# Optimization experiments

Hardware: AMD Instinct MI355X
Metric: run time of the kernel (lower is better)

The kernel has to match this reference:

```python
import jax, jax.numpy as jnp
import numpy as np

N, D_IN, FC_DIM, GROUP, NONGT, EMB = 4096, 12544, 1024, 16, 300, 64
DG = FC_DIM // GROUP  # 64 per-head dim


def extract_position_matrix(bbox, nongt_dim):
    xmin, ymin, xmax, ymax = jnp.split(bbox, 4, axis=1)  # each [N,1]
    bw = xmax - xmin + 1.0
    bh = ymax - ymin + 1.0
    cx = 0.5 * (xmin + xmax)
    cy = 0.5 * (ymin + ymax)
    dx = jnp.log(jnp.maximum(jnp.abs((cx - cx.T) / bw), 1e-3))
    dy = jnp.log(jnp.maximum(jnp.abs((cy - cy.T) / bh), 1e-3))
    dw = jnp.log(bw / bw.T)
    dh = jnp.log(bh / bh.T)
    # slice to first nongt_dim columns, stack -> [N, nongt, 4]
    return jnp.stack([dx[:, :nongt_dim], dy[:, :nongt_dim],
                      dw[:, :nongt_dim], dh[:, :nongt_dim]], axis=2)


def extract_position_embedding(pos_mat, feat_dim=64, wave_length=1000.0):
    n8 = feat_dim // 8
    feat_range = jnp.arange(n8, dtype=pos_mat.dtype)
    dim_mat = wave_length ** (8.0 / feat_dim * feat_range)  # [8]
    div = 100.0 * pos_mat[..., None] / dim_mat              # [N,nongt,4,8]
    emb = jnp.concatenate([jnp.sin(div), jnp.cos(div)], axis=3)  # [N,nongt,4,16]
    return emb.reshape(pos_mat.shape[0], pos_mat.shape[1], feat_dim)


def attention_multi_head(feat, pos_emb, Wpos, bpos, Wq, bq, Wk, bk, Wo, bo):
    # feat: [N, 1024], pos_emb: [N, nongt, 64]
    nongt_feat = feat[:NONGT]                                   # [nongt, 1024]
    aff_w = jax.nn.relu(pos_emb @ Wpos + bpos)                  # [N, nongt, G]
    aff_w = jnp.swapaxes(aff_w, 1, 2)                           # [N, G, nongt]
    q = (feat @ Wq + bq).reshape(-1, GROUP, DG)                 # [N, G, dg]
    k = (nongt_feat @ Wk + bk).reshape(NONGT, GROUP, DG)        # [nongt, G, dg]
    aff = jnp.einsum('ngd,mgd->ngm', q, k) * (1.0 / np.sqrt(DG))  # [N, G, nongt]
    logits = jnp.log(jnp.maximum(aff_w, 1e-6)) + aff
    p = jax.nn.softmax(logits, axis=2)                          # [N, G, nongt]
    out = jnp.einsum('ngm,mc->ngc', p, nongt_feat)              # [N, G, 1024]
    # grouped 1x1 conv: group g maps 1024 -> 64 outputs
    lin = jnp.einsum('ngc,goc->ngo', out, Wo) + bo.reshape(GROUP, DG)
    return lin.reshape(feat.shape[0], FC_DIM)


def setup_inputs() -> dict:
    key = jax.random.key(0)
    ks = jax.random.split(key, 20)
    roi_feat = jax.random.normal(ks[0], (N, D_IN), dtype=jnp.float32)
    u = jax.random.uniform(ks[1], (N, 4), dtype=jnp.float32)
    x1 = u[:, 0:1] * 500.0
    y1 = u[:, 1:2] * 500.0
    bbox = jnp.concatenate([x1, y1, x1 + u[:, 2:3] * 200.0 + 1.0,
                            y1 + u[:, 3:4] * 200.0 + 1.0], axis=1)
    def lin(k, fin, fout):
        s = 1.0 / np.sqrt(fin)
        return jax.random.normal(k, (fin, fout), dtype=jnp.float32) * s
    inp = {'roi_feat': roi_feat, 'bbox': bbox,
           'W_fc1': lin(ks[2], D_IN, FC_DIM), 'b_fc1': jnp.zeros((FC_DIM,), jnp.float32),
           'W_fc2': lin(ks[3], FC_DIM, FC_DIM), 'b_fc2': jnp.zeros((FC_DIM,), jnp.float32)}
    for i, base in [(1, 4), (2, 10)]:
        inp[f'Wpos{i}'] = lin(ks[base], EMB, GROUP)
        inp[f'bpos{i}'] = jnp.zeros((GROUP,), jnp.float32)
        inp[f'Wq{i}'] = lin(ks[base + 1], FC_DIM, FC_DIM)
        inp[f'bq{i}'] = jnp.zeros((FC_DIM,), jnp.float32)
        inp[f'Wk{i}'] = lin(ks[base + 2], FC_DIM, FC_DIM)
        inp[f'bk{i}'] = jnp.zeros((FC_DIM,), jnp.float32)
        inp[f'Wo{i}'] = jax.random.normal(ks[base + 3], (GROUP, DG, FC_DIM), dtype=jnp.float32) * (1.0 / np.sqrt(FC_DIM))
        inp[f'bo{i}'] = jnp.zeros((FC_DIM,), jnp.float32)
    return inp


def reference(roi_feat, bbox, W_fc1, b_fc1, W_fc2, b_fc2,
              Wpos1, bpos1, Wq1, bq1, Wk1, bk1, Wo1, bo1,
              Wpos2, bpos2, Wq2, bq2, Wk2, bk2, Wo2, bo2):
    pos_mat = extract_position_matrix(bbox, NONGT)
    pos_emb = extract_position_embedding(pos_mat, EMB)
    x = roi_feat
    for (Wf, bf, Wp, bp, Wq, bq, Wk, bk, Wo, bo) in [
        (W_fc1, b_fc1, Wpos1, bpos1, Wq1, bq1, Wk1, bk1, Wo1, bo1),
        (W_fc2, b_fc2, Wpos2, bpos2, Wq2, bq2, Wk2, bk2, Wo2, bo2)]:
        x = x @ Wf + bf
        attn = attention_multi_head(x, pos_emb, Wp, bp, Wq, bq, Wk, bk, Wo, bo)
        x = jax.nn.relu(x + attn)
    return x
```

## Files before the change

### kernel.cpp

```cpp
#include <hip/hip_runtime.h>


using bf16x8 = __attribute__((ext_vector_type(8))) short;
using u16x4  = __attribute__((ext_vector_type(4))) short;
using f32x4  = __attribute__((ext_vector_type(4))) float;
typedef unsigned short u16;
typedef unsigned int   u32;

#define DEV __device__ __forceinline__

DEV u16 f2bf(float f) {
  u32 u = __float_as_uint(f);
  return (u16)((u + 0x7FFFu + ((u >> 16) & 1u)) >> 16);
}
DEV float bf2f(u16 h) { return __uint_as_float(((u32)h) << 16); }

DEV f32x4 mfma16(bf16x8 a, bf16x8 b, f32x4 c) {
  return __builtin_amdgcn_mfma_f32_16x16x32_bf16(a, b, c, 0, 0, 0);
}
DEV void gload16(const u16* g, u16* l) {
  __builtin_amdgcn_global_load_lds((const __attribute__((address_space(1))) void*)g,
                                   (__attribute__((address_space(3))) void*)l, 16, 0, 0);
}

DEV void fsincos(float x, float* s, float* c) {
  float r = x * 0.15915494309189535f;
  r -= rintf(r);
  float a = r * 6.283185307179586f;
  *s = __sinf(a); *c = __cosf(a);
}

struct PrepArgs {
  const float* Wo1; u16* Wo1_b;
  const float* Wo2; u16* Wo2_b;
  const float* Wfc1; u16* Wfc1_t;
  const float* wsrc[5]; u16* wdst[5];
};

__global__ __launch_bounds__(256) void prep_kernel(PrepArgs p) {
  __shared__ float tp[32][36];
  int b = blockIdx.x, tid = threadIdx.x;
  if (b < 1024) {
    const float* src = (b < 512) ? p.Wo1 : p.Wo2;
    u16* dst = (b < 512) ? p.Wo1_b : p.Wo2_b;
    size_t i = ((size_t)(b & 511) * 256 + tid) * 8;
    float4 a = *(const float4*)(src + i);
    float4 c = *(const float4*)(src + i + 4);
    bf16x8 v;
    v[0]=(short)f2bf(a.x); v[1]=(short)f2bf(a.y); v[2]=(short)f2bf(a.z); v[3]=(short)f2bf(a.w);
    v[4]=(short)f2bf(c.x); v[5]=(short)f2bf(c.y); v[6]=(short)f2bf(c.z); v[7]=(short)f2bf(c.w);
    *(bf16x8*)(dst + i) = v;
    return;
  }
  const float* in; u16* out; int r0, c0, R, C;
  if (b < 13568) {
    int idx = b - 1024;
    in = p.Wfc1; out = p.Wfc1_t; R = 12544; C = 1024;
    r0 = (idx >> 5) * 32; c0 = (idx & 31) * 32;
  } else {
    int idx = b - 13568;
    int z = idx >> 10, rest = idx & 1023;
    in = p.wsrc[z]; out = p.wdst[z]; R = 1024; C = 1024;
    r0 = (rest >> 5) * 32; c0 = (rest & 31) * 32;
  }
  {
    int r = tid >> 3, c4 = (tid & 7) * 4;
    float4 v = *(const float4*)(in + (size_t)(r0 + r) * C + c0 + c4);
    *(float4*)&tp[r][c4] = v;
  }
  __syncthreads();
  {
    int c = tid >> 3, r4 = (tid & 7) * 4;
    u16x4 o;
    o[0] = (short)f2bf(tp[r4 + 0][c]); o[1] = (short)f2bf(tp[r4 + 1][c]);
    o[2] = (short)f2bf(tp[r4 + 2][c]); o[3] = (short)f2bf(tp[r4 + 3][c]);
    *(u16x4*)(out + (size_t)(c0 + c) * R + r0 + r4) = o;
  }
}

__global__ __launch_bounds__(512, 2) void gemm8p(
    const float* __restrict__ A, const u16* __restrict__ Bt,
    float* __restrict__ P) {
  const int K = 12544;
  __shared__ u16 lds[65536];
  int tid = threadIdx.x;
  int w = tid >> 6, l = tid & 63, h = l >> 4, l15 = l & 15;
  int wm = w >> 2, wn = w & 3;

  int b = ((blockIdx.x & 7) << 5) | (blockIdx.x >> 3);
  int bz = b >> 6, rest = b & 63;
  int bm = (rest & 15) * 256;
  int bn = (rest >> 4) * 256;
  size_t k0 = (size_t)bz * 3136;

  int arow = tid >> 3;
  int c0 = (tid & 7) * 8;
  const float* pA0 = A + (size_t)(bm + arow) * K + k0 + c0;
  const size_t aseg = (size_t)64 * K;
  int awe = ((arow * 128 + c0 * 2) ^ ((arow & 7) << 4)) >> 1;

  int X = ((tid >> 3) & 7) << 4;
  int lb2 = (tid * 16) ^ X;
  int lr = lb2 >> 7, lc = (lb2 & 127) >> 1;
  const u16* pB = Bt + (size_t)(bn + lr) * K + k0 + lc;
  const size_t o64 = (size_t)64 * K, o128 = (size_t)128 * K, o192 = (size_t)192 * K;

  int swz = (l15 & 7) << 3;
  int xk0 = (h * 8) ^ swz;
  int xk1 = 32 ^ xk0;
  int rA = (wm * 64 + l15) * 64;
  int rB = (wn * 32 + l15) * 64;

  f32x4 acc[8][4];
#pragma unroll
  for (int i = 0; i < 8; i++)
#pragma unroll
    for (int j = 0; j < 4; j++) acc[i][j] = (f32x4){0.f, 0.f, 0.f, 0.f};

  float4 a0[4], a1[4];
  bf16x8 af[4][2], bl[2][2], bh[2][2];

#define AISSUE(kk) { _Pragma("unroll") for (int s = 0; s < 4; s++) {     \
    a0[s] = *(const float4*)(pA0 + s * aseg + (kk));                     \
    a1[s] = *(const float4*)(pA0 + s * aseg + (kk) + 4); } }
#define BISSUE_LO(WB, kk) {                                              \
    gload16(pB + (kk),        (WB) + tid * 8);                           \
    gload16(pB + o64 + (kk),  (WB) + 4096 + tid * 8); }
#define BISSUE_HI(WB, kk) {                                              \
    gload16(pB + o128 + (kk), (WB) + 8192 + tid * 8);                    \
    gload16(pB + o192 + (kk), (WB) + 12288 + tid * 8); }
#define AWRITE(WA) { _Pragma("unroll") for (int s = 0; s < 4; s++) {     \
    bf16x8 v;                                                            \
    v[0]=(short)f2bf(a0[s].x); v[1]=(short)f2bf(a0[s].y);                \
    v[2]=(short)f2bf(a0[s].z); v[3]=(short)f2bf(a0[s].w);                \
    v[4]=(short)f2bf(a1[s].x); v[5]=(short)f2bf(a1[s].y);                \
    v[6]=(short)f2bf(a1[s].z); v[7]=(short)f2bf(a1[s].w);                \
    *(bf16x8*)&(WA)[awe + s * 4096] = v; } }
#define READ_AF(BASE)                                                    \
  _Pragma("unroll") for (int i = 0; i < 4; i++) {                        \
    af[i][0] = *(const bf16x8*)&LA[(BASE) + rA + i * 1024 + xk0];        \
    af[i][1] = *(const bf16x8*)&LA[(BASE) + rA + i * 1024 + xk1];        \
  }
#define READ_BL {                                                        \
  _Pragma("unroll") for (int j = 0; j < 2; j++) {                        \
    bl[j][0] = *(const bf16x8*)&LB[rB + j * 1024 + xk0];                 \
    bl[j][1] = *(const bf16x8*)&LB[rB + j * 1024 + xk1]; } }
#define READ_BH {                                                        \
  _Pragma("unroll") for (int j = 0; j < 2; j++) {                        \
    bh[j][0] = *(const bf16x8*)&LB[8192 + rB + j * 1024 + xk0];          \
    bh[j][1] = *(const bf16x8*)&LB[8192 + rB + j * 1024 + xk1]; } }
#define Q_MFMA(QR, QC, BF)                                               \
  __builtin_amdgcn_s_setprio(1);                                         \
  _Pragma("unroll") for (int i = 0; i < 4; i++)                          \
    _Pragma("unroll") for (int j = 0; j < 2; j++) {                      \
      acc[(QR)*4+i][(QC)*2+j] = mfma16(af[i][0], BF[j][0], acc[(QR)*4+i][(QC)*2+j]); \
      acc[(QR)*4+i][(QC)*2+j] = mfma16(af[i][1], BF[j][1], acc[(QR)*4+i][(QC)*2+j]); \
    }                                                                    \
  __builtin_amdgcn_s_setprio(0);
#define SBAR __builtin_amdgcn_sched_barrier(0)

  AISSUE(0);
  BISSUE_LO(lds + 16384, 0);
  BISSUE_HI(lds + 16384, 0);
  AWRITE(lds);
  asm volatile("s_waitcnt vmcnt(0) lgkmcnt(0)" ::: "memory");
  __builtin_amdgcn_s_barrier();

  for (int t = 0; t < 48; t++) {
    const u16* LA = lds + (t & 1) * 32768;
    const u16* LB = LA + 16384;
    u16* WA = lds + ((t + 1) & 1) * 32768;
    u16* WB = WA + 16384;
    int ktn = (t + 1) * 64;
    AISSUE(ktn);
    asm volatile("s_waitcnt vmcnt(10) lgkmcnt(0)" ::: "memory");
    __builtin_amdgcn_s_barrier();
    SBAR;
    READ_AF(0);
    READ_BL;
    Q_MFMA(0, 0, bl);
    SBAR;
    BISSUE_LO(WB, ktn);
    asm volatile("s_waitcnt vmcnt(10)" ::: "memory");
    __builtin_amdgcn_s_barrier();
    SBAR;
    READ_BH;
    Q_MFMA(0, 1, bh);
    SBAR;
    BISSUE_HI(WB, ktn);
    READ_AF(8192);
    Q_MFMA(1, 1, bh);
    SBAR;
    Q_MFMA(1, 0, bl);
    SBAR;
    AWRITE(WA);
  }
  {
    const u16* LA = lds;
    const u16* LB = lds + 16384;
    asm volatile("s_waitcnt vmcnt(2) lgkmcnt(0)" ::: "memory");
    __builtin_amdgcn_s_barrier();
    SBAR;
    READ_AF(0);
    READ_BL;
    Q_MFMA(0, 0, bl);
    SBAR;
    asm volatile("s_waitcnt vmcnt(0)" ::: "memory");
    __builtin_amdgcn_s_barrier();
    SBAR;
    READ_BH;
    Q_MFMA(0, 1, bh);
    SBAR;
    READ_AF(8192);
    Q_MFMA(1, 1, bh);
    Q_MFMA(1, 0, bl);
  }
#undef AISSUE
#undef BISSUE_LO
#undef BISSUE_HI
#undef AWRITE
#undef READ_AF
#undef READ_BL
#undef READ_BH
#undef Q_MFMA
#undef SBAR

  float* dst = P + (size_t)bz * 4096 * 1024;
#pragma unroll
  for (int qr = 0; qr < 2; qr++)
#pragma unroll
    for (int i = 0; i < 4; i++)
#pragma unroll
      for (int qc = 0; qc < 2; qc++)
#pragma unroll
        for (int j = 0; j < 2; j++) {
          int row0 = bm + qr * 128 + wm * 64 + i * 16 + h * 4;
          int col  = bn + qc * 128 + wn * 32 + j * 16 + l15;
          f32x4 v = acc[qr * 4 + i][qc * 2 + j];
#pragma unroll
          for (int r = 0; r < 4; r++)
            dst[(size_t)(row0 + r) * 1024 + col] = v[r];
        }
}

__constant__ float C100D[8] = {100.f, 42.16965034285822f, 17.78279410038923f,
                               7.498942093324559f, 3.1622776601683795f,
                               1.333521432163324f, 0.5623413251903491f,
                               0.23713737056616552f};

__global__ __launch_bounds__(256) void reduce_pos_kernel(
    const float* __restrict__ P, const float* __restrict__ bias,
    float* __restrict__ xf, u16* __restrict__ xb,
    const float* __restrict__ bbox,
    const float* __restrict__ Wpos1, const float* __restrict__ Wpos2,
    const float* __restrict__ bpos1, const float* __restrict__ bpos2,
    u16* __restrict__ logw1, u16* __restrict__ logw2) {
  __shared__ u16 pool[18944];
  int tid = threadIdx.x;
  if (blockIdx.x < 2048) {
    const size_t MN = (size_t)4096 * 1024;
    size_t i = ((size_t)blockIdx.x * 256 + tid) * 4;
    size_t stride = (size_t)2048 * 256 * 4;
    for (; i < MN; i += stride) {
      float4 a = *(const float4*)(P + i);
      float4 b = *(const float4*)(P + MN + i);
      float4 c = *(const float4*)(P + 2 * MN + i);
      float4 d = *(const float4*)(P + 3 * MN + i);
      float4 bv = *(const float4*)(bias + (i & 1023));
      float4 r;
      r.x = a.x + b.x + c.x + d.x + bv.x;
      r.y = a.y + b.y + c.y + d.y + bv.y;
      r.z = a.z + b.z + c.z + d.z + bv.z;
      r.w = a.w + b.w + c.w + d.w + bv.w;
      *(float4*)(xf + i) = r;
      u16x4 hv;
      hv[0] = (short)f2bf(r.x); hv[1] = (short)f2bf(r.y);
      hv[2] = (short)f2bf(r.z); hv[3] = (short)f2bf(r.w);
      *(u16x4*)(xb + i) = hv;
    }
    return;
  }
  u16* emb_s = pool;
  u16* wp_s  = pool + 5632;
  u16* lw_s  = pool + 8448;
  int n = blockIdx.x - 2048;
  int w = tid >> 6, l = tid & 63, h = l >> 4, l15 = l & 15;
  for (int idx = tid; idx < 1024; idx += 256) {
    int e = idx >> 4, c = idx & 15;
    wp_s[c * 88 + e]        = f2bf(Wpos1[idx]);
    wp_s[(16 + c) * 88 + e] = f2bf(Wpos2[idx]);
  }
  float4 bn = ((const float4*)bbox)[n];
  float bw_n = bn.z - bn.x + 1.f, bh_n = bn.w - bn.y + 1.f;
  float cx_n = 0.5f * (bn.x + bn.z), cy_n = 0.5f * (bn.y + bn.w);
  float bps0 = bpos1[l15], bps1 = bpos2[l15];
  int p = tid >> 2, k = tid & 3;

  for (int m0 = 0; m0 < 320; m0 += 64) {
    int m = m0 + p;
    float4 bm = ((const float4*)bbox)[m];
    float v;
    if (k == 0)      v = logf(fmaxf(fabsf((cx_n - 0.5f * (bm.x + bm.z)) / bw_n), 1e-3f));
    else if (k == 1) v = logf(fmaxf(fabsf((cy_n - 0.5f * (bm.y + bm.w)) / bh_n), 1e-3f));
    else if (k == 2) v = logf(bw_n / (bm.z - bm.x + 1.f));
    else             v = logf(bh_n / (bm.w - bm.y + 1.f));
    __syncthreads();
#pragma unroll
    for (int tt = 0; tt < 8; tt++) {
      float s, c; fsincos(v * C100D[tt], &s, &c);
      emb_s[p * 88 + k * 16 + tt]     = f2bf(s);
      emb_s[p * 88 + k * 16 + 8 + tt] = f2bf(c);
    }
    __syncthreads();
    f32x4 acc0 = {0.f, 0.f, 0.f, 0.f}, acc1 = {0.f, 0.f, 0.f, 0.f};
    bf16x8 a0 = *(const bf16x8*)&emb_s[(w * 16 + l15) * 88 + h * 8];
    bf16x8 a1 = *(const bf16x8*)&emb_s[(w * 16 + l15) * 88 + 32 + h * 8];
    bf16x8 b00 = *(const bf16x8*)&wp_s[l15 * 88 + h * 8];
    bf16x8 b01 = *(const bf16x8*)&wp_s[l15 * 88 + 32 + h * 8];
    bf16x8 b10 = *(const bf16x8*)&wp_s[(16 + l15) * 88 + h * 8];
    bf16x8 b11 = *(const bf16x8*)&wp_s[(16 + l15) * 88 + 32 + h * 8];
    acc0 = mfma16(a0, b00, acc0); acc0 = mfma16(a1, b01, acc0);
    acc1 = mfma16(a0, b10, acc1); acc1 = mfma16(a1, b11, acc1);
#pragma unroll
    for (int r = 0; r < 4; r++) {
      int mm = m0 + w * 16 + h * 4 + r;
      lw_s[l15 * 328 + mm]        = f2bf(logf(fmaxf(acc0[r] + bps0, 1e-6f)));
      lw_s[(16 + l15) * 328 + mm] = f2bf(logf(fmaxf(acc1[r] + bps1, 1e-6f)));
    }
  }
  __syncthreads();
  for (int i = tid; i < 1280; i += 256) {
    int layer = i / 640, rest = i - layer * 640;
    int gg = rest / 40, seg = rest - gg * 40;
    bf16x8 v = *(const bf16x8*)&lw_s[(layer * 16 + gg) * 328 + seg * 8];
    u16* dst = (layer ? logw2 : logw1) + ((size_t)gg * 4096 + n) * 320 + seg * 8;
    *(bf16x8*)dst = v;
  }
}

struct GDesc {
  const u16* A; const u16* Bt; const float* bias;
  u16* Cb; float* Cf;
  int M, N, K, ldc, nt;
};

__global__ __launch_bounds__(256, 2) void gemmU(GDesc g0, GDesc g1, GDesc g2,
                                                int c0, int c1) {
  __shared__ u16 lds[32768];
  GDesc g; int lb = blockIdx.x;
  if (lb < c0) { g = g0; lb = (lb & 7) * (c0 >> 3) + (lb >> 3); }
  else if (lb < c1) { g = g1; lb -= c0; }
  else { g = g2; lb -= c1; }
  int bm = (lb / g.nt) * 128, bn = (lb % g.nt) * 128;
  int tid = threadIdx.x;
  int w = tid >> 6, l = tid & 63, h = l >> 4, l15 = l & 15;
  int wm = w >> 1, wn = w & 1;
  int K = g.K;

  int X = ((tid >> 3) & 7) << 4;
  int lbyte = (tid * 16) ^ X;
  int lr = lbyte >> 7, lc = (lbyte & 127) >> 1;
  const u16 *pa[4], *pb[4];
#pragma unroll
  for (int c = 0; c < 4; c++) {
    pa[c] = g.A  + (size_t)min(bm + c * 32 + lr, g.M - 1) * K + lc;
    pb[c] = g.Bt + (size_t)min(bn + c * 32 + lr, g.N - 1) * K + lc;
  }

  int swz = (l15 & 7) << 3;
  int xk0 = (h * 8) ^ swz;
  int xk1 = 32 ^ xk0;
  int rA = (wm * 64 + l15) * 64;
  int rB = (wn * 64 + l15) * 64;

  f32x4 acc[4][4];
#pragma unroll
  for (int i = 0; i < 4; i++)
#pragma unroll
    for (int j = 0; j < 4; j++) acc[i][j] = (f32x4){0.f, 0.f, 0.f, 0.f};

#define ISSUEU(W, kk)                                     \
  { gload16(pa[0] + (kk), (W) + tid * 8);                 \
    gload16(pa[1] + (kk), (W) + 2048 + tid * 8);          \
    gload16(pa[2] + (kk), (W) + 4096 + tid * 8);          \
    gload16(pa[3] + (kk), (W) + 6144 + tid * 8);          \
    gload16(pb[0] + (kk), (W) + 8192 + tid * 8);          \
    gload16(pb[1] + (kk), (W) + 10240 + tid * 8);         \
    gload16(pb[2] + (kk), (W) + 12288 + tid * 8);         \
    gload16(pb[3] + (kk), (W) + 14336 + tid * 8); }

  ISSUEU(lds, 0);
  int ktiles = K >> 6;
  for (int t = 0; t < ktiles; t++) {
    const u16* LA = lds + (t & 1) * 16384;
    const u16* LB = LA + 8192;
    u16* W = lds + ((t ^ 1) & 1) * 16384;
    if (t < ktiles - 1) {
      ISSUEU(W, (t + 1) * 64);
      asm volatile("s_waitcnt vmcnt(8)" ::: "memory");
    } else {
      asm volatile("s_waitcnt vmcnt(0)" ::: "memory");
    }
    __builtin_amdgcn_s_barrier();
    asm volatile("" ::: "memory");
    bf16x8 a[4][2], bfr[4][2];
#pragma unroll
    for (int i = 0; i < 4; i++) {
      a[i][0] = *(const bf16x8*)&LA[rA + i * 1024 + xk0];
      a[i][1] = *(const bf16x8*)&LA[rA + i * 1024 + xk1];
    }
#pragma unroll
    for (int j = 0; j < 4; j++) {
      bfr[j][0] = *(const bf16x8*)&LB[rB + j * 1024 + xk0];
      bfr[j][1] = *(const bf16x8*)&LB[rB + j * 1024 + xk1];
    }
    __builtin_amdgcn_s_setprio(1);
#pragma unroll
    for (int i = 0; i < 4; i++)
#pragma unroll
      for (int j = 0; j < 4; j++) {
        acc[i][j] = mfma16(a[i][0], bfr[j][0], acc[i][j]);
        acc[i][j] = mfma16(a[i][1], bfr[j][1], acc[i][j]);
      }
    __builtin_amdgcn_s_setprio(0);
    asm volatile("" ::: "memory");
    __builtin_amdgcn_s_barrier();
  }
#undef ISSUEU

#pragma unroll
  for (int i = 0; i < 4; i++) {
#pragma unroll
    for (int j = 0; j < 4; j++) {
      int col = bn + wn * 64 + j * 16 + l15;
      if (col >= g.ldc) continue;
      float bv = (g.bias != nullptr && col < g.N) ? g.bias[col] : 0.f;
      int row0 = bm + wm * 64 + i * 16 + h * 4;
#pragma unroll
      for (int r = 0; r < 4; r++) {
        int row = row0 + r;
        if (row >= g.M) continue;
        float v = acc[i][j][r] + bv;
        size_t off = (size_t)row * g.ldc + col;
        g.Cb[off] = f2bf(v);
        if (g.Cf != nullptr) g.Cf[off] = v;
      }
    }
  }
}

template <bool LAST>
__global__ __launch_bounds__(256) void attn_kernel(
    const u16* __restrict__ qb, const u16* __restrict__ kb,
    const u16* __restrict__ kvt, const u16* __restrict__ logw,
    const float* __restrict__ xf, const float* __restrict__ bo,
    float* __restrict__ outf, u16* __restrict__ outb) {
  __shared__ u16 ps[64 * 344];
  int tid = threadIdx.x;
  int g = blockIdx.y, n0 = blockIdx.x * 64;
  int w = tid >> 6, l = tid & 63, h = l >> 4, l15 = l & 15;

  {
    const u16* src = logw + ((size_t)g * 4096 + n0) * 320;
    for (int i = tid; i < 64 * 40; i += 256) {
      int row = i / 40, seg = i - row * 40;
      *(bf16x8*)&ps[row * 328 + seg * 8] = *(const bf16x8*)(src + row * 320 + seg * 8);
    }
  }
  int nrow = n0 + w * 16 + l15;
  const u16* qp = qb + (size_t)nrow * 1024 + g * 64;
  bf16x8 aq0 = *(const bf16x8*)(qp + h * 8);
  bf16x8 aq1 = *(const bf16x8*)(qp + 32 + h * 8);

  f32x4 acc[19];
#pragma unroll
  for (int f = 0; f < 19; f++) acc[f] = (f32x4){0.f, 0.f, 0.f, 0.f};
  const u16* kp = kb + g * 64 + h * 8;
#pragma unroll
  for (int f = 0; f < 19; f++) {
    bf16x8 b0 = *(const bf16x8*)(kp + (size_t)(f * 16 + l15) * 1024);
    bf16x8 b1 = *(const bf16x8*)(kp + (size_t)(f * 16 + l15) * 1024 + 32);
    acc[f] = mfma16(aq0, b0, acc[f]);
    acc[f] = mfma16(aq1, b1, acc[f]);
  }
  __syncthreads();

  int nbase = n0 + w * 16 + h * 4;
  int lrow = w * 16 + h * 4;
  float mx[4] = {-INFINITY, -INFINITY, -INFINITY, -INFINITY};
  float sm[4] = {0.f, 0.f, 0.f, 0.f};
#pragma unroll
  for (int f = 0; f < 19; f++) {
    int m = f * 16 + l15;
#pragma unroll
    for (int r = 0; r < 4; r++) {
      float lw = -INFINITY;
      if (m < 300) lw = bf2f(ps[(lrow + r) * 328 + m]);
      float lg = acc[f][r] * 0.125f + lw;
      acc[f][r] = lg;
      mx[r] = fmaxf(mx[r], lg);
    }
  }
#pragma unroll
  for (int d = 1; d < 16; d <<= 1)
#pragma unroll
    for (int r = 0; r < 4; r++) mx[r] = fmaxf(mx[r], __shfl_xor(mx[r], d));
#pragma unroll
  for (int f = 0; f < 19; f++)
#pragma unroll
    for (int r = 0; r < 4; r++) {
      float p = __expf(acc[f][r] - mx[r]);
      acc[f][r] = p; sm[r] += p;
    }
#pragma unroll
  for (int d = 1; d < 16; d <<= 1)
#pragma unroll
    for (int r = 0; r < 4; r++) sm[r] += __shfl_xor(sm[r], d);
  float inv[4];
#pragma unroll
  for (int r = 0; r < 4; r++) inv[r] = 1.f / sm[r];

  __syncthreads();
#pragma unroll
  for (int f = 0; f < 19; f++)
#pragma unroll
    for (int r = 0; r < 4; r++)
      ps[(lrow + r) * 344 + f * 16 + l15] = f2bf(acc[f][r]);
#pragma unroll
  for (int r = 0; r < 4; r++)
    ps[(lrow + r) * 344 + 304 + l15] = 0;

  f32x4 acc2[4];
#pragma unroll
  for (int fo = 0; fo < 4; fo++) acc2[fo] = (f32x4){0.f, 0.f, 0.f, 0.f};
  const u16* vp = kvt + (size_t)g * 64 * 320 + h * 8;
#pragma unroll
  for (int ks = 0; ks < 10; ks++) {
    bf16x8 ap = *(const bf16x8*)&ps[(w * 16 + l15) * 344 + ks * 32 + h * 8];
#pragma unroll
    for (int fo = 0; fo < 4; fo++) {
      bf16x8 bv = *(const bf16x8*)(vp + (size_t)(fo * 16 + l15) * 320 + ks * 32);
      acc2[fo] = mfma16(ap, bv, acc2[fo]);
    }
  }
#pragma unroll
  for (int fo = 0; fo < 4; fo++) {
    int col = g * 64 + fo * 16 + l15;
    float bov = bo[col];
#pragma unroll
    for (int r = 0; r < 4; r++) {
      int row = nbase + r;
      float v = xf[(size_t)row * 1024 + col] + acc2[fo][r] * inv[r] + bov;
      v = fmaxf(v, 0.f);
      if (LAST) outf[(size_t)row * 1024 + col] = v;
      else      outb[(size_t)row * 1024 + col] = f2bf(v);
    }
  }
}

extern "C" void kernel_launch(void* const* d_in, const int* in_sizes, int n_in,
                              void* d_out, int out_size, void* d_ws, size_t ws_size,
                              hipStream_t stream) {
  (void)in_sizes; (void)n_in; (void)out_size; (void)ws_size;
  const float* roi   = (const float*)d_in[0];
  const float* bbox  = (const float*)d_in[1];
  const float* Wfc1  = (const float*)d_in[2];
  const float* bfc1  = (const float*)d_in[3];
  const float* Wfc2  = (const float*)d_in[4];
  const float* bfc2  = (const float*)d_in[5];
  const float* Wpos1 = (const float*)d_in[6];
  const float* bpos1 = (const float*)d_in[7];
  const float* Wq1   = (const float*)d_in[8];
  const float* bq1   = (const float*)d_in[9];
  const float* Wk1   = (const float*)d_in[10];
  const float* bk1   = (const float*)d_in[11];
  const float* Wo1   = (const float*)d_in[12];
  const float* bo1   = (const float*)d_in[13];
  const float* Wpos2 = (const float*)d_in[14];
  const float* bpos2 = (const float*)d_in[15];
  const float* Wq2   = (const float*)d_in[16];
  const float* bq2   = (const float*)d_in[17];
  const float* Wk2   = (const float*)d_in[18];
  const float* bk2   = (const float*)d_in[19];
  const float* Wo2   = (const float*)d_in[20];
  const float* bo2   = (const float*)d_in[21];

  char* ws = (char*)d_ws;
  u16*  Wfc1_t = (u16*)(ws + 102760448);
  u16*  Wfc2_t = (u16*)(ws + 128450560);
  u16*  Wq1_t  = (u16*)(ws + 130547712);
  u16*  Wk1_t  = (u16*)(ws + 132644864);
  u16*  Wq2_t  = (u16*)(ws + 134742016);
  u16*  Wk2_t  = (u16*)(ws + 136839168);
  u16*  Wo1_b  = (u16*)(ws + 138936320);
  u16*  Wo2_b  = (u16*)(ws + 141033472);
  float* Pp    = (float*)(ws + 143134720);
  float* xf    = (float*)(ws + 227020800);
  u16*  xb_f   = (u16*)(ws + 243798016);
  u16*  xb_a   = (u16*)(ws + 252186624);
  u16*  q_b    = (u16*)(ws + 260575232);
  u16*  k_b    = (u16*)(ws + 268963840);
  u16*  kvt_b  = (u16*)(ws + 269578240);
  u16*  logw1  = (u16*)(ws + 270233600);
  u16*  logw2  = (u16*)(ws + 312176640);

  {
    PrepArgs p;
    p.Wo1 = Wo1;   p.Wo1_b = Wo1_b;
    p.Wo2 = Wo2;   p.Wo2_b = Wo2_b;
    p.Wfc1 = Wfc1; p.Wfc1_t = Wfc1_t;
    p.wsrc[0] = Wfc2; p.wdst[0] = Wfc2_t;
    p.wsrc[1] = Wq1;  p.wdst[1] = Wq1_t;
    p.wsrc[2] = Wk1;  p.wdst[2] = Wk1_t;
    p.wsrc[3] = Wq2;  p.wdst[3] = Wq2_t;
    p.wsrc[4] = Wk2;  p.wdst[4] = Wk2_t;
    prep_kernel<<<18688, 256, 0, stream>>>(p);
  }
  gemm8p<<<256, 512, 0, stream>>>(roi, Wfc1_t, Pp);
  reduce_pos_kernel<<<6144, 256, 0, stream>>>(Pp, bfc1, xf, xb_f, bbox,
                                              Wpos1, Wpos2, bpos1, bpos2,
                                              logw1, logw2);
  {
    GDesc q  = {xb_f,  Wq1_t, bq1, q_b,   nullptr, 4096, 1024, 1024, 1024, 8};
    GDesc kk = {xb_f,  Wk1_t, bk1, k_b,   nullptr,  300, 1024, 1024, 1024, 8};
    GDesc kv = {Wo1_b, xb_f,  nullptr, kvt_b, nullptr, 1024, 300, 1024, 320, 3};
    gemmU<<<304, 256, 0, stream>>>(q, kk, kv, 256, 280);
  }
  attn_kernel<false><<<dim3(64, 16), 256, 0, stream>>>(q_b, k_b, kvt_b, logw1, xf, bo1, nullptr, xb_a);

  {
    GDesc fc = {xb_a, Wfc2_t, bfc2, xb_f, xf, 4096, 1024, 1024, 1024, 8};
    gemmU<<<256, 256, 0, stream>>>(fc, fc, fc, 256, 256);
  }
  {
    GDesc q  = {xb_f,  Wq2_t, bq2, q_b,   nullptr, 4096, 1024, 1024, 1024, 8};
    GDesc kk = {xb_f,  Wk2_t, bk2, k_b,   nullptr,  300, 1024, 1024, 1024, 8};
    GDesc kv = {Wo2_b, xb_f,  nullptr, kvt_b, nullptr, 1024, 300, 1024, 320, 3};
    gemmU<<<304, 256, 0, stream>>>(q, kk, kv, 256, 280);
  }
  attn_kernel<true><<<dim3(64, 16), 256, 0, stream>>>(q_b, k_b, kvt_b, logw2, xf, bo2, (float*)d_out, nullptr);
}
```

Before: 409.6 us.

## Load B fragments directly from global into registers, stage only A in LDS

The big FC GEMM no longer stages the bf16 weight tile (B) through LDS. Each wave now reads its B fragments straight from global memory into registers, and only the converted A tile is double-buffered in LDS, which halves the LDS footprint. The wave layout changes from 2x4 to 4x2 with 64x128 per-wave tiles, and the hand-tuned vmcnt split-barrier pipeline is replaced by a plain __syncthreads loop. Each B fragment is now fetched by every wave row that uses it, adding global/L2 traffic, and global-load latency is exposed directly before the MFMAs.

```diff
diff --git a/kernel.cpp b/kernel.cpp
--- a/kernel.cpp
+++ b/kernel.cpp
@@ -82,10 +82,10 @@
     const float* __restrict__ A, const u16* __restrict__ Bt,
     float* __restrict__ P) {
   const int K = 12544;
-  __shared__ u16 lds[65536];
+  __shared__ u16 lds[32768];
   int tid = threadIdx.x;
   int w = tid >> 6, l = tid & 63, h = l >> 4, l15 = l & 15;
-  int wm = w >> 2, wn = w & 3;
+  int wm = w >> 1, wn = w & 1;
 
   int b = ((blockIdx.x & 7) << 5) | (blockIdx.x >> 3);
   int bz = b >> 6, rest = b & 63;
@@ -99,36 +99,24 @@
   const size_t aseg = (size_t)64 * K;
   int awe = ((arow * 128 + c0 * 2) ^ ((arow & 7) << 4)) >> 1;
 
-  int X = ((tid >> 3) & 7) << 4;
-  int lb2 = (tid * 16) ^ X;
-  int lr = lb2 >> 7, lc = (lb2 & 127) >> 1;
-  const u16* pB = Bt + (size_t)(bn + lr) * K + k0 + lc;
-  const size_t o64 = (size_t)64 * K, o128 = (size_t)128 * K, o192 = (size_t)192 * K;
-
   int swz = (l15 & 7) << 3;
   int xk0 = (h * 8) ^ swz;
   int xk1 = 32 ^ xk0;
   int rA = (wm * 64 + l15) * 64;
-  int rB = (wn * 32 + l15) * 64;
-
-  f32x4 acc[8][4];
-#pragma unroll
-  for (int i = 0; i < 8; i++)
-#pragma unroll
-    for (int j = 0; j < 4; j++) acc[i][j] = (f32x4){0.f, 0.f, 0.f, 0.f};
+
+  const u16* pBf = Bt + (size_t)(bn + wn * 128 + l15) * K + k0 + h * 8;
+
+  f32x4 acc[4][8];
+#pragma unroll
+  for (int i = 0; i < 4; i++)
+#pragma unroll
+    for (int j = 0; j < 8; j++) acc[i][j] = (f32x4){0.f, 0.f, 0.f, 0.f};
 
   float4 a0[4], a1[4];
-  bf16x8 af[4][2], bl[2][2], bh[2][2];
 
 #define AISSUE(kk) { _Pragma("unroll") for (int s = 0; s < 4; s++) {     \
     a0[s] = *(const float4*)(pA0 + s * aseg + (kk));                     \
     a1[s] = *(const float4*)(pA0 + s * aseg + (kk) + 4); } }
-#define BISSUE_LO(WB, kk) {                                              \
-    gload16(pB + (kk),        (WB) + tid * 8);                           \
-    gload16(pB + o64 + (kk),  (WB) + 4096 + tid * 8); }
-#define BISSUE_HI(WB, kk) {                                              \
-    gload16(pB + o128 + (kk), (WB) + 8192 + tid * 8);                    \
-    gload16(pB + o192 + (kk), (WB) + 12288 + tid * 8); }
 #define AWRITE(WA) { _Pragma("unroll") for (int s = 0; s < 4; s++) {     \
     bf16x8 v;                                                            \
     v[0]=(short)f2bf(a0[s].x); v[1]=(short)f2bf(a0[s].y);                \
@@ -136,111 +124,69 @@
     v[4]=(short)f2bf(a1[s].x); v[5]=(short)f2bf(a1[s].y);                \
     v[6]=(short)f2bf(a1[s].z); v[7]=(short)f2bf(a1[s].w);                \
     *(bf16x8*)&(WA)[awe + s * 4096] = v; } }
-#define READ_AF(BASE)                                                    \
-  _Pragma("unroll") for (int i = 0; i < 4; i++) {                        \
-    af[i][0] = *(const bf16x8*)&LA[(BASE) + rA + i * 1024 + xk0];        \
-    af[i][1] = *(const bf16x8*)&LA[(BASE) + rA + i * 1024 + xk1];        \
-  }
-#define READ_BL {                                                        \
-  _Pragma("unroll") for (int j = 0; j < 2; j++) {                        \
-    bl[j][0] = *(const bf16x8*)&LB[rB + j * 1024 + xk0];                 \
-    bl[j][1] = *(const bf16x8*)&LB[rB + j * 1024 + xk1]; } }
-#define READ_BH {                                                        \
-  _Pragma("unroll") for (int j = 0; j < 2; j++) {                        \
-    bh[j][0] = *(const bf16x8*)&LB[8192 + rB + j * 1024 + xk0];          \
-    bh[j][1] = *(const bf16x8*)&LB[8192 + rB + j * 1024 + xk1]; } }
-#define Q_MFMA(QR, QC, BF)                                               \
+#define LOADB(dst, jc, kt) { _Pragma("unroll") for (int jj = 0; jj < 2; jj++) { \
+    const u16* bp = pBf + (size_t)((jc) * 2 + jj) * 16 * K + (kt);       \
+    dst[jj][0] = *(const bf16x8*)bp;                                     \
+    dst[jj][1] = *(const bf16x8*)(bp + 32); } }
+#define CLUST(jc, B)                                                     \
   __builtin_amdgcn_s_setprio(1);                                         \
   _Pragma("unroll") for (int i = 0; i < 4; i++)                          \
-    _Pragma("unroll") for (int j = 0; j < 2; j++) {                      \
-      acc[(QR)*4+i][(QC)*2+j] = mfma16(af[i][0], BF[j][0], acc[(QR)*4+i][(QC)*2+j]); \
-      acc[(QR)*4+i][(QC)*2+j] = mfma16(af[i][1], BF[j][1], acc[(QR)*4+i][(QC)*2+j]); \
+    _Pragma("unroll") for (int jj = 0; jj < 2; jj++) {                   \
+      acc[i][(jc)*2+jj] = mfma16(af[i][0], B[jj][0], acc[i][(jc)*2+jj]); \
+      acc[i][(jc)*2+jj] = mfma16(af[i][1], B[jj][1], acc[i][(jc)*2+jj]); \
     }                                                                    \
   __builtin_amdgcn_s_setprio(0);
 #define SBAR __builtin_amdgcn_sched_barrier(0)
 
   AISSUE(0);
-  BISSUE_LO(lds + 16384, 0);
-  BISSUE_HI(lds + 16384, 0);
   AWRITE(lds);
-  asm volatile("s_waitcnt vmcnt(0) lgkmcnt(0)" ::: "memory");
-  __builtin_amdgcn_s_barrier();
-
-  for (int t = 0; t < 48; t++) {
-    const u16* LA = lds + (t & 1) * 32768;
-    const u16* LB = LA + 16384;
-    u16* WA = lds + ((t + 1) & 1) * 32768;
-    u16* WB = WA + 16384;
-    int ktn = (t + 1) * 64;
-    AISSUE(ktn);
-    asm volatile("s_waitcnt vmcnt(10) lgkmcnt(0)" ::: "memory");
-    __builtin_amdgcn_s_barrier();
+  __syncthreads();
+
+  for (int t = 0; t < 49; t++) {
+    const u16* LA = lds + (t & 1) * 16384;
+    u16* WA = lds + ((t + 1) & 1) * 16384;
+    int kt = t * 64;
+    if (t < 48) AISSUE(kt + 64);
+    bf16x8 af[4][2];
+#pragma unroll
+    for (int i = 0; i < 4; i++) {
+      af[i][0] = *(const bf16x8*)&LA[rA + i * 1024 + xk0];
+      af[i][1] = *(const bf16x8*)&LA[rA + i * 1024 + xk1];
+    }
+    bf16x8 b0[2][2], b1[2][2];
+    LOADB(b0, 0, kt);
+    LOADB(b1, 1, kt);
+    CLUST(0, b0);
     SBAR;
-    READ_AF(0);
-    READ_BL;
-    Q_MFMA(0, 0, bl);
+    LOADB(b0, 2, kt);
+    CLUST(1, b1);
     SBAR;
-    BISSUE_LO(WB, ktn);
-    asm volatile("s_waitcnt vmcnt(10)" ::: "memory");
-    __builtin_amdgcn_s_barrier();
+    LOADB(b1, 3, kt);
+    CLUST(2, b0);
     SBAR;
-    READ_BH;
-    Q_MFMA(0, 1, bh);
+    CLUST(3, b1);
     SBAR;
-    BISSUE_HI(WB, ktn);
-    READ_AF(8192);
-    Q_MFMA(1, 1, bh);
-    SBAR;
-    Q_MFMA(1, 0, bl);
-    SBAR;
-    AWRITE(WA);
-  }
-  {
-    const u16* LA = lds;
-    const u16* LB = lds + 16384;
-    asm volatile("s_waitcnt vmcnt(2) lgkmcnt(0)" ::: "memory");
-    __builtin_amdgcn_s_barrier();
-    SBAR;
-    READ_AF(0);
-    READ_BL;
-    Q_MFMA(0, 0, bl);
-    SBAR;
-    asm volatile("s_waitcnt vmcnt(0)" ::: "memory");
-    __builtin_amdgcn_s_barrier();
-    SBAR;
-    READ_BH;
-    Q_MFMA(0, 1, bh);
-    SBAR;
-    READ_AF(8192);
-    Q_MFMA(1, 1, bh);
-    Q_MFMA(1, 0, bl);
+    if (t < 48) AWRITE(WA);
+    __syncthreads();
   }
 #undef AISSUE
-#undef BISSUE_LO
-#undef BISSUE_HI
 #undef AWRITE
-#undef READ_AF
-#undef READ_BL
-#undef READ_BH
-#undef Q_MFMA
+#undef LOADB
+#undef CLUST
 #undef SBAR
 
   float* dst = P + (size_t)bz * 4096 * 1024;
 #pragma unroll
-  for (int qr = 0; qr < 2; qr++)
-#pragma unroll
-    for (int i = 0; i < 4; i++)
-#pragma unroll
-      for (int qc = 0; qc < 2; qc++)
-#pragma unroll
-        for (int j = 0; j < 2; j++) {
-          int row0 = bm + qr * 128 + wm * 64 + i * 16 + h * 4;
-          int col  = bn + qc * 128 + wn * 32 + j * 16 + l15;
-          f32x4 v = acc[qr * 4 + i][qc * 2 + j];
-#pragma unroll
-          for (int r = 0; r < 4; r++)
-            dst[(size_t)(row0 + r) * 1024 + col] = v[r];
-        }
+  for (int i = 0; i < 4; i++)
+#pragma unroll
+    for (int j = 0; j < 8; j++) {
+      int row0 = bm + wm * 64 + i * 16 + h * 4;
+      int col  = bn + wn * 128 + j * 16 + l15;
+      f32x4 v = acc[i][j];
+#pragma unroll
+      for (int r = 0; r < 4; r++)
+        dst[(size_t)(row0 + r) * 1024 + col] = v[r];
+    }
 }
 
 __constant__ float C100D[8] = {100.f, 42.16965034285822f, 17.78279410038923f,
```

Measured after the change: 540.2 us. 31.9% more time.
